# Kernel tuning notes

Measured on AMD Instinct MI355X. Metric: run time of the kernel, lower is better.

The kernel has to match this reference:

```python
import jax, jax.numpy as jnp
import numpy as np

L, B, S, H, V = 6, 8, 2048, 768, 32000
FF = 4 * H
EPS = 1e-5


def _ln(x, g, b):
    m = x.mean(-1, keepdims=True)
    v = ((x - m) ** 2).mean(-1, keepdims=True)
    return (x - m) / jnp.sqrt(v + EPS) * g + b


def setup_inputs() -> dict:
    key = jax.random.key(0)
    ks = iter(jax.random.split(key, 32))
    std = 0.02
    n = lambda shape: jax.random.normal(next(ks), shape, dtype=jnp.float32) * std
    inp = {
        'input_ids': jax.random.randint(next(ks), (B, S), 0, V, dtype=jnp.int64),
        'attention_mask': jnp.ones((B, S), dtype=jnp.int32),
        'tok_emb': n((V, H)),
        'pos_emb': n((S, H)),
        'Wq': n((L, H, H)), 'bq': n((L, H)),
        'Wk': n((L, H, H)), 'bk': n((L, H)),
        'Wv': n((L, H, H)), 'bv': n((L, H)),
        'Wo': n((L, H, H)), 'bo': n((L, H)),
        'ln1_g': jnp.ones((L, H), jnp.float32), 'ln1_b': jnp.zeros((L, H), jnp.float32),
        'ln2_g': jnp.ones((L, H), jnp.float32), 'ln2_b': jnp.zeros((L, H), jnp.float32),
        'W1': n((L, H, FF)), 'b1': n((L, FF)),
        'W2': n((L, FF, H)), 'b2': n((L, H)),
        'fln_g': jnp.ones((H,), jnp.float32), 'fln_b': jnp.zeros((H,), jnp.float32),
        'cls_W': n((H, 1)), 'cls_b': n((1,)),
    }
    return inp


def reference(input_ids, attention_mask, tok_emb, pos_emb, Wq, bq, Wk, bk, Wv, bv,
              Wo, bo, ln1_g, ln1_b, ln2_g, ln2_b, W1, b1, W2, b2,
              fln_g, fln_b, cls_W, cls_b):
    x = tok_emb[input_ids] + pos_emb[None, :S, :]  # [B,S,H]
    causal = jnp.triu(jnp.ones((S, S), dtype=bool), 1)  # True above diagonal
    pad = ~(attention_mask.astype(bool))[:, None, :]    # [B,1,S] True where padded
    full_mask = causal[None, :, :] | pad                # [B,S,S]
    scale = 1.0 / (H ** 0.5)
    for i in range(L):
        # --- attention block (pre-LN) ---
        h = _ln(x, ln1_g[i], ln1_b[i])
        q = h @ Wq[i] + bq[i]
        k = h @ Wk[i] + bk[i]
        v = h @ Wv[i] + bv[i]
        scores = jnp.einsum('bqd,bkd->bqk', q, k) * scale
        scores = jnp.where(full_mask, -jnp.inf, scores)
        attn = jax.nn.softmax(scores, axis=-1)
        o = jnp.einsum('bqk,bkd->bqd', attn, v) @ Wo[i] + bo[i]
        x = o + x
        # --- FFN block ---
        h = _ln(x, ln2_g[i], ln2_b[i])
        x = jax.nn.gelu(h @ W1[i] + b1[i], approximate=False) @ W2[i] + b2[i] + x
    x = _ln(x, fln_g, fln_b)
    # select hidden state of last non-padded token per row
    m = attention_mask.astype(jnp.int32)
    last = m.sum(1) - 1                      # [B]
    x_last = x[jnp.arange(B), last]          # [B,H]
    logits = x_last @ cls_W + cls_b          # [B,1]
    return logits
```

## Files before the change

### kernel.cpp

```cpp
#include <hip/hip_runtime.h>
#include <hip/hip_bf16.h>

#define Bn 8
#define Sn 2048
#define Hn 768
#define FFn 3072
#define Ln 6
#define BSn (Bn * Sn)
#define CQ 512
#define LN_EPS 1e-5f

typedef __hip_bfloat16 bf16;
typedef __bf16 bf16x8 __attribute__((ext_vector_type(8)));
typedef float f32x4 __attribute__((ext_vector_type(4)));

__device__ __forceinline__ float b2f(bf16 v) { return __bfloat162float(v); }
__device__ __forceinline__ void stc(float* p, float v) { *p = v; }
__device__ __forceinline__ void stc(bf16* p, float v) { *p = __float2bfloat16(v); }

union Pk8 { float4 v; bf16 h[8]; };

__device__ __forceinline__ void gld16(const bf16* g, short* l) {
  __builtin_amdgcn_global_load_lds(
      (const __attribute__((address_space(1))) unsigned int*)g,
      (__attribute__((address_space(3))) unsigned int*)l, 16, 0, 0);
}

__global__ void __launch_bounds__(256) embed_kernel(
    const int* __restrict__ ids, const float* __restrict__ tok,
    const float* __restrict__ pos, float* __restrict__ x) {
  long t = blockIdx.x;
  int s = (int)(t & (Sn - 1));
  long id = ids[t];
  const float* tr = tok + id * Hn;
  const float* pr = pos + (long)s * Hn;
  float* xr = x + t * Hn;
  for (int d = threadIdx.x; d < Hn; d += 256)
    xr[d] = tr[d] + pr[d];
}

__global__ void __launch_bounds__(256) transpose_cvt_kernel(
    const float* __restrict__ W, bf16* __restrict__ Wt, int K, int N) {
  __shared__ float t[32][33];
  int n0 = blockIdx.x * 32, k0 = blockIdx.y * 32;
  int tx = threadIdx.x & 31, ty = threadIdx.x >> 5;
#pragma unroll
  for (int i = 0; i < 32; i += 8)
    t[ty + i][tx] = W[(long)(k0 + ty + i) * N + n0 + tx];
  __syncthreads();
#pragma unroll
  for (int i = 0; i < 32; i += 8)
    stc(Wt + (long)(n0 + ty + i) * K + k0 + tx, t[tx][ty + i]);
}

__global__ void __launch_bounds__(256) ln_kernel(
    const float* __restrict__ x, const float* __restrict__ g,
    const float* __restrict__ b, bf16* __restrict__ out) {
  long token = blockIdx.x;
  const float* xr = x + token * Hn;
  bf16* orow = out + token * Hn;
  int tid = threadIdx.x;

  float vals[3];
  float s1 = 0.f;
#pragma unroll
  for (int i = 0; i < 3; i++) {
    vals[i] = xr[tid + 256 * i];
    s1 += vals[i];
  }
  __shared__ float sb[4];
  __shared__ float stat[2];
#pragma unroll
  for (int off = 32; off > 0; off >>= 1) s1 += __shfl_down(s1, off, 64);
  if ((tid & 63) == 0) sb[tid >> 6] = s1;
  __syncthreads();
  if (tid == 0) stat[0] = (sb[0] + sb[1] + sb[2] + sb[3]) * (1.0f / Hn);
  __syncthreads();
  float mean = stat[0];

  float s2 = 0.f;
#pragma unroll
  for (int i = 0; i < 3; i++) {
    float d = vals[i] - mean;
    s2 += d * d;
  }
#pragma unroll
  for (int off = 32; off > 0; off >>= 1) s2 += __shfl_down(s2, off, 64);
  if ((tid & 63) == 0) sb[tid >> 6] = s2;
  __syncthreads();
  if (tid == 0)
    stat[1] = rsqrtf((sb[0] + sb[1] + sb[2] + sb[3]) * (1.0f / Hn) + LN_EPS);
  __syncthreads();
  float inv = stat[1];

#pragma unroll
  for (int i = 0; i < 3; i++) {
    int d = tid + 256 * i;
    stc(orow + d, (vals[i] - mean) * inv * g[d] + b[d]);
  }
}

template <int EPI, typename CT>
__global__ void __launch_bounds__(256) mfma_gemm_kernel(
    const bf16* __restrict__ A, const bf16* __restrict__ Bt,
    const float* __restrict__ bias, const float* __restrict__ res,
    CT* __restrict__ C, int M, int N, int K) {
  __shared__ short As[128 * 32];
  __shared__ short Bs[128 * 32];
  int tid = threadIdx.x;
  int wave = tid >> 6, lane = tid & 63;
  int waveM = wave >> 1, waveN = wave & 1;
  int quad = lane >> 4, l16 = lane & 15;
  long rowBase = (long)blockIdx.y * 128;
  long colBase = (long)blockIdx.x * 128;
  const bf16* Ag = A + rowBase * K;
  const bf16* Bg = Bt + colBase * K;

  int srow = lane >> 2;
  int schunk = (lane & 3) * 8;

  f32x4 acc[4][4] = {};

  for (int kt = 0; kt < K; kt += 32) {
#pragma unroll
    for (int c = 0; c < 2; c++) {
      int r0 = wave * 32 + c * 16;
      gld16(Ag + (long)(r0 + srow) * K + kt + schunk, &As[r0 * 32]);
      gld16(Bg + (long)(r0 + srow) * K + kt + schunk, &Bs[r0 * 32]);
    }
    __syncthreads();

    bf16x8 af[4], bfr[4];
#pragma unroll
    for (int t = 0; t < 4; t++)
      af[t] = *(const bf16x8*)&As[(waveM * 64 + t * 16 + l16) * 32 + quad * 8];
#pragma unroll
    for (int u = 0; u < 4; u++)
      bfr[u] = *(const bf16x8*)&Bs[(waveN * 64 + u * 16 + l16) * 32 + quad * 8];
#pragma unroll
    for (int t = 0; t < 4; t++)
#pragma unroll
      for (int u = 0; u < 4; u++)
        acc[t][u] = __builtin_amdgcn_mfma_f32_16x16x32_bf16(af[t], bfr[u],
                                                            acc[t][u], 0, 0, 0);
    __syncthreads();
  }

#pragma unroll
  for (int t = 0; t < 4; t++) {
#pragma unroll
    for (int u = 0; u < 4; u++) {
      int col = (int)colBase + waveN * 64 + u * 16 + l16;
      float bv = bias[col];
      if (EPI == 3) {
        union { uint2 w; bf16 h[4]; } pk;
        long row0 = rowBase + waveM * 64 + t * 16 + quad * 4;
        long bb = row0 >> 11;
        long s = row0 & (Sn - 1);
#pragma unroll
        for (int r = 0; r < 4; r++)
          pk.h[r] = __float2bfloat16(acc[t][u][r] + bv);
        *reinterpret_cast<uint2*>((bf16*)C + (bb * Hn + col) * Sn + s) = pk.w;
      } else {
#pragma unroll
        for (int r = 0; r < 4; r++) {
          long row = rowBase + waveM * 64 + t * 16 + quad * 4 + r;
          float v = acc[t][u][r] + bv;
          if (EPI == 1) v += res[row * N + col];
          if (EPI == 2) v = 0.5f * v * (1.0f + erff(v * 0.70710678118654752f));
          stc(C + row * N + col, v);
        }
      }
    }
  }
}

__global__ void __launch_bounds__(256) qk_mfma_kernel(
    const bf16* __restrict__ q, const bf16* __restrict__ k,
    bf16* __restrict__ sc, int q0) {
  int kBase = blockIdx.x * 128;
  int qBase = q0 + blockIdx.y * 128;
  if (kBase > qBase + 127) return;
  int b = blockIdx.z;
  const bf16* Ag = q + ((long)b * Sn + qBase) * Hn;
  const bf16* Bg = k + ((long)b * Sn + kBase) * Hn;

  __shared__ short As[128 * 32];
  __shared__ short Bs[128 * 32];
  int tid = threadIdx.x;
  int wave = tid >> 6, lane = tid & 63;
  int waveM = wave >> 1, waveN = wave & 1;
  int quad = lane >> 4, l16 = lane & 15;
  int srow = lane >> 2;
  int schunk = (lane & 3) * 8;

  f32x4 acc[4][4] = {};

  for (int kt = 0; kt < Hn; kt += 32) {
#pragma unroll
    for (int c = 0; c < 2; c++) {
      int r0 = wave * 32 + c * 16;
      gld16(Ag + (long)(r0 + srow) * Hn + kt + schunk, &As[r0 * 32]);
      gld16(Bg + (long)(r0 + srow) * Hn + kt + schunk, &Bs[r0 * 32]);
    }
    __syncthreads();

    bf16x8 af[4], bfr[4];
#pragma unroll
    for (int t = 0; t < 4; t++)
      af[t] = *(const bf16x8*)&As[(waveM * 64 + t * 16 + l16) * 32 + quad * 8];
#pragma unroll
    for (int u = 0; u < 4; u++)
      bfr[u] = *(const bf16x8*)&Bs[(waveN * 64 + u * 16 + l16) * 32 + quad * 8];
#pragma unroll
    for (int t = 0; t < 4; t++)
#pragma unroll
      for (int u = 0; u < 4; u++)
        acc[t][u] = __builtin_amdgcn_mfma_f32_16x16x32_bf16(af[t], bfr[u],
                                                            acc[t][u], 0, 0, 0);
    __syncthreads();
  }

  const float scale = 0.03608439182435161f;
#pragma unroll
  for (int t = 0; t < 4; t++)
#pragma unroll
    for (int u = 0; u < 4; u++) {
      int col = kBase + waveN * 64 + u * 16 + l16;
#pragma unroll
      for (int r = 0; r < 4; r++) {
        long qRel = (long)(qBase - q0) + waveM * 64 + t * 16 + quad * 4 + r;
        stc(sc + ((long)b * CQ + qRel) * Sn + col, acc[t][u][r] * scale);
      }
    }
}

__global__ void __launch_bounds__(256) pv_mfma_kernel(
    const bf16* __restrict__ p, const bf16* __restrict__ vT,
    bf16* __restrict__ o, int q0) {
  int colBase = blockIdx.x * 128;
  int qBase = q0 + blockIdx.y * 128;
  int b = blockIdx.z;
  int klimit = qBase + 128;
  const bf16* Ag = p + ((long)b * CQ + (qBase - q0)) * Sn;
  const bf16* Bg = vT + ((long)b * Hn + colBase) * Sn;

  __shared__ short As[128 * 32];
  __shared__ short Bs[128 * 32];
  int tid = threadIdx.x;
  int wave = tid >> 6, lane = tid & 63;
  int waveM = wave >> 1, waveN = wave & 1;
  int quad = lane >> 4, l16 = lane & 15;
  int srow = lane >> 2;
  int schunk = (lane & 3) * 8;

  f32x4 acc[4][4] = {};

  for (int kt = 0; kt < klimit; kt += 32) {
#pragma unroll
    for (int c = 0; c < 2; c++) {
      int r0 = wave * 32 + c * 16;
      gld16(Ag + (long)(r0 + srow) * Sn + kt + schunk, &As[r0 * 32]);
      gld16(Bg + (long)(r0 + srow) * Sn + kt + schunk, &Bs[r0 * 32]);
    }
    __syncthreads();

    bf16x8 af[4], bfr[4];
#pragma unroll
    for (int t = 0; t < 4; t++)
      af[t] = *(const bf16x8*)&As[(waveM * 64 + t * 16 + l16) * 32 + quad * 8];
#pragma unroll
    for (int u = 0; u < 4; u++)
      bfr[u] = *(const bf16x8*)&Bs[(waveN * 64 + u * 16 + l16) * 32 + quad * 8];
#pragma unroll
    for (int t = 0; t < 4; t++)
#pragma unroll
      for (int u = 0; u < 4; u++)
        acc[t][u] = __builtin_amdgcn_mfma_f32_16x16x32_bf16(af[t], bfr[u],
                                                            acc[t][u], 0, 0, 0);
    __syncthreads();
  }

#pragma unroll
  for (int t = 0; t < 4; t++)
#pragma unroll
    for (int u = 0; u < 4; u++) {
      int col = colBase + waveN * 64 + u * 16 + l16;
#pragma unroll
      for (int r = 0; r < 4; r++) {
        long qAbs = (long)qBase + waveM * 64 + t * 16 + quad * 4 + r;
        stc(o + ((long)b * Sn + qAbs) * Hn + col, acc[t][u][r]);
      }
    }
}

__global__ void __launch_bounds__(256) softmax_kernel(
    bf16* __restrict__ sc, const int* __restrict__ mask, int q0) {
  int qRel = blockIdx.x;
  int b = blockIdx.y;
  int qg = q0 + qRel;
  bf16* row = sc + ((long)b * CQ + qRel) * Sn;
  const int* mrow = mask + b * Sn;
  int tid = threadIdx.x;
  int n = qg + 1;
  int limit = (qg & ~127) + 128;

  float sv[8];
  float lmax = -1e30f;
#pragma unroll
  for (int it = 0; it < 8; it++) {
    int kk = tid + it * 256;
    float s = -1e30f;
    if (kk < n) {
      s = b2f(row[kk]);
      if (mrow[kk] == 0) s = -1e30f;
    }
    sv[it] = s;
    lmax = fmaxf(lmax, s);
  }
  __shared__ float sb[4];
  __shared__ float stat;
#pragma unroll
  for (int off = 32; off > 0; off >>= 1)
    lmax = fmaxf(lmax, __shfl_down(lmax, off, 64));
  if ((tid & 63) == 0) sb[tid >> 6] = lmax;
  __syncthreads();
  if (tid == 0) stat = fmaxf(fmaxf(sb[0], sb[1]), fmaxf(sb[2], sb[3]));
  __syncthreads();
  float gmax = stat;

  float ev[8];
  float lsum = 0.f;
#pragma unroll
  for (int it = 0; it < 8; it++) {
    int kk = tid + it * 256;
    float e = 0.f;
    if (kk < n) e = __expf(sv[it] - gmax);
    ev[it] = e;
    lsum += e;
  }
#pragma unroll
  for (int off = 32; off > 0; off >>= 1) lsum += __shfl_down(lsum, off, 64);
  if ((tid & 63) == 0) sb[tid >> 6] = lsum;
  __syncthreads();
  if (tid == 0) stat = sb[0] + sb[1] + sb[2] + sb[3];
  __syncthreads();
  float inv = 1.0f / stat;

#pragma unroll
  for (int it = 0; it < 8; it++) {
    int kk = tid + it * 256;
    if (kk < n)
      stc(row + kk, ev[it] * inv);
    else if (kk < limit)
      stc(row + kk, 0.f);
  }
}

__global__ void __launch_bounds__(256) cls_kernel(
    const bf16* __restrict__ h, const int* __restrict__ mask,
    const float* __restrict__ clsW, const float* __restrict__ clsb,
    float* __restrict__ out) {
  int b = blockIdx.x;
  int tid = threadIdx.x;
  __shared__ float sb[4];
  __shared__ int ib[4];
  __shared__ int lastsh;

  int ls = 0;
  for (int s = tid; s < Sn; s += 256) ls += mask[b * Sn + s];
#pragma unroll
  for (int off = 32; off > 0; off >>= 1) ls += __shfl_down(ls, off, 64);
  if ((tid & 63) == 0) ib[tid >> 6] = ls;
  __syncthreads();
  if (tid == 0) lastsh = ib[0] + ib[1] + ib[2] + ib[3] - 1;
  __syncthreads();
  int last = lastsh;

  const bf16* row = h + ((long)b * Sn + last) * Hn;
  float acc = 0.f;
  for (int d = tid; d < Hn; d += 256) acc += b2f(row[d]) * clsW[d];
#pragma unroll
  for (int off = 32; off > 0; off >>= 1) acc += __shfl_down(acc, off, 64);
  if ((tid & 63) == 0) sb[tid >> 6] = acc;
  __syncthreads();
  if (tid == 0) out[b] = sb[0] + sb[1] + sb[2] + sb[3] + clsb[0];
}

extern "C" void kernel_launch(void* const* d_in, const int* in_sizes, int n_in,
                              void* d_out, int out_size, void* d_ws,
                              size_t ws_size, hipStream_t stream) {
  const int* ids     = (const int*)d_in[0];
  const int* mask    = (const int*)d_in[1];
  const float* tok   = (const float*)d_in[2];
  const float* pos   = (const float*)d_in[3];
  const float* Wq    = (const float*)d_in[4];
  const float* bq    = (const float*)d_in[5];
  const float* Wk    = (const float*)d_in[6];
  const float* bk    = (const float*)d_in[7];
  const float* Wv    = (const float*)d_in[8];
  const float* bv    = (const float*)d_in[9];
  const float* Wo    = (const float*)d_in[10];
  const float* bo    = (const float*)d_in[11];
  const float* ln1g  = (const float*)d_in[12];
  const float* ln1b  = (const float*)d_in[13];
  const float* ln2g  = (const float*)d_in[14];
  const float* ln2b  = (const float*)d_in[15];
  const float* W1    = (const float*)d_in[16];
  const float* b1    = (const float*)d_in[17];
  const float* W2    = (const float*)d_in[18];
  const float* b2    = (const float*)d_in[19];
  const float* flng  = (const float*)d_in[20];
  const float* flnb  = (const float*)d_in[21];
  const float* clsW  = (const float*)d_in[22];
  const float* clsb  = (const float*)d_in[23];

  float* x = (float*)d_ws;
  bf16* h  = (bf16*)(x + (size_t)BSn * Hn);
  bf16* cb = h + (size_t)BSn * Hn;
  bf16* qb = cb;
  bf16* kb = cb + (size_t)BSn * Hn;
  bf16* vtb = cb + 2 * (size_t)BSn * Hn;
  bf16* scb = cb + 3 * (size_t)BSn * Hn;
  bf16* wt = cb + (size_t)BSn * FFn;
  bf16* wqT = wt;
  bf16* wkT = wqT + (size_t)Hn * Hn;
  bf16* wvT = wkT + (size_t)Hn * Hn;
  bf16* woT = wvT + (size_t)Hn * Hn;
  bf16* w1T = woT + (size_t)Hn * Hn;
  bf16* w2T = w1T + (size_t)Hn * FFn;

  const int M = BSn;
  dim3 blk(256);
  dim3 gridH128(Hn / 128, M / 128);
  dim3 gridF128(FFn / 128, M / 128);
  dim3 gridQK(Sn / 128, CQ / 128, Bn);
  dim3 gridSM(CQ, Bn);
  dim3 gridPV(Hn / 128, CQ / 128, Bn);
  dim3 gridTH(Hn / 32, Hn / 32);
  dim3 gridT1(FFn / 32, Hn / 32);
  dim3 gridT2(Hn / 32, FFn / 32);

  embed_kernel<<<BSn, blk, 0, stream>>>(ids, tok, pos, x);

  for (int l = 0; l < Ln; l++) {
    const float* Wq_l = Wq + (size_t)l * Hn * Hn;
    const float* Wk_l = Wk + (size_t)l * Hn * Hn;
    const float* Wv_l = Wv + (size_t)l * Hn * Hn;
    const float* Wo_l = Wo + (size_t)l * Hn * Hn;
    const float* W1_l = W1 + (size_t)l * Hn * FFn;
    const float* W2_l = W2 + (size_t)l * FFn * Hn;

    transpose_cvt_kernel<<<gridTH, blk, 0, stream>>>(Wq_l, wqT, Hn, Hn);
    transpose_cvt_kernel<<<gridTH, blk, 0, stream>>>(Wk_l, wkT, Hn, Hn);
    transpose_cvt_kernel<<<gridTH, blk, 0, stream>>>(Wv_l, wvT, Hn, Hn);
    transpose_cvt_kernel<<<gridTH, blk, 0, stream>>>(Wo_l, woT, Hn, Hn);
    transpose_cvt_kernel<<<gridT1, blk, 0, stream>>>(W1_l, w1T, Hn, FFn);
    transpose_cvt_kernel<<<gridT2, blk, 0, stream>>>(W2_l, w2T, FFn, Hn);

    ln_kernel<<<BSn, blk, 0, stream>>>(x, ln1g + l * Hn, ln1b + l * Hn, h);
    mfma_gemm_kernel<0, bf16><<<gridH128, blk, 0, stream>>>(
        h, wqT, bq + l * Hn, nullptr, qb, M, Hn, Hn);
    mfma_gemm_kernel<0, bf16><<<gridH128, blk, 0, stream>>>(
        h, wkT, bk + l * Hn, nullptr, kb, M, Hn, Hn);
    mfma_gemm_kernel<3, bf16><<<gridH128, blk, 0, stream>>>(
        h, wvT, bv + l * Hn, nullptr, vtb, M, Hn, Hn);
    for (int c = 0; c < Sn / CQ; c++) {
      int q0 = c * CQ;
      qk_mfma_kernel<<<gridQK, blk, 0, stream>>>(qb, kb, scb, q0);
      softmax_kernel<<<gridSM, blk, 0, stream>>>(scb, mask, q0);
      pv_mfma_kernel<<<gridPV, blk, 0, stream>>>(scb, vtb, h, q0);
    }
    mfma_gemm_kernel<1, float><<<gridH128, blk, 0, stream>>>(
        h, woT, bo + l * Hn, x, x, M, Hn, Hn);

    ln_kernel<<<BSn, blk, 0, stream>>>(x, ln2g + l * Hn, ln2b + l * Hn, h);
    mfma_gemm_kernel<2, bf16><<<gridF128, blk, 0, stream>>>(
        h, w1T, b1 + l * FFn, nullptr, cb, M, FFn, Hn);
    mfma_gemm_kernel<1, float><<<gridH128, blk, 0, stream>>>(
        cb, w2T, b2 + l * Hn, x, x, M, Hn, FFn);
  }

  ln_kernel<<<BSn, blk, 0, stream>>>(x, flng, flnb, h);
  cls_kernel<<<Bn, blk, 0, stream>>>(h, mask, clsW, clsb, (float*)d_out);
}
```

Measured before the change: 4.729 ms.

## Fuse QKV GEMMs and weight transposes, add XCD-aware tile remap, vectorize softmax

Merges the six per-layer weight transpose launches into one kernel, and fuses the Q, K and V projections into a single GEMM over a concatenated transposed weight. The epilogue routes each output column range to the q, k or transposed-v buffer with the matching bias. GEMM launches switch to a 1D grid with a remap that gives each XCD a contiguous run of tiles, aiming for better L2 reuse. Softmax now loads and stores 8 bf16 values per thread with vector accesses. Risks are wrong offsets in the fused epilogue layout and added index arithmetic.

```diff
diff --git a/kernel.cpp b/kernel.cpp
--- a/kernel.cpp
+++ b/kernel.cpp
@@ -39,10 +39,35 @@
     xr[d] = tr[d] + pr[d];
 }
 
-__global__ void __launch_bounds__(256) transpose_cvt_kernel(
-    const float* __restrict__ W, bf16* __restrict__ Wt, int K, int N) {
+__global__ void __launch_bounds__(256) transpose_all_kernel(
+    const float* __restrict__ Wq_l, const float* __restrict__ Wk_l,
+    const float* __restrict__ Wv_l, const float* __restrict__ Wo_l,
+    const float* __restrict__ W1_l, const float* __restrict__ W2_l,
+    bf16* __restrict__ wt) {
+  int id = blockIdx.x;
+  const float* W;
+  bf16* Wt;
+  int K, N, tile, tilesX;
+  if (id < 2304) {
+    int w = id / 576;
+    tile = id - w * 576;
+    W = (w == 0) ? Wq_l : (w == 1) ? Wk_l : (w == 2) ? Wv_l : Wo_l;
+    Wt = wt + (size_t)w * Hn * Hn;
+    K = Hn; N = Hn; tilesX = Hn / 32;
+  } else if (id < 4608) {
+    tile = id - 2304;
+    W = W1_l;
+    Wt = wt + 4 * (size_t)Hn * Hn;
+    K = Hn; N = FFn; tilesX = FFn / 32;
+  } else {
+    tile = id - 4608;
+    W = W2_l;
+    Wt = wt + 4 * (size_t)Hn * Hn + (size_t)Hn * FFn;
+    K = FFn; N = Hn; tilesX = Hn / 32;
+  }
+  int n0 = (tile % tilesX) * 32, k0 = (tile / tilesX) * 32;
+
   __shared__ float t[32][33];
-  int n0 = blockIdx.x * 32, k0 = blockIdx.y * 32;
   int tx = threadIdx.x & 31, ty = threadIdx.x >> 5;
 #pragma unroll
   for (int i = 0; i < 32; i += 8)
@@ -104,15 +129,24 @@
 __global__ void __launch_bounds__(256) mfma_gemm_kernel(
     const bf16* __restrict__ A, const bf16* __restrict__ Bt,
     const float* __restrict__ bias, const float* __restrict__ res,
-    CT* __restrict__ C, int M, int N, int K) {
+    CT* __restrict__ C, int M, int N, int K,
+    const float* __restrict__ bias2, const float* __restrict__ bias3) {
   __shared__ short As[128 * 32];
   __shared__ short Bs[128 * 32];
   int tid = threadIdx.x;
   int wave = tid >> 6, lane = tid & 63;
   int waveM = wave >> 1, waveN = wave & 1;
   int quad = lane >> 4, l16 = lane & 15;
-  long rowBase = (long)blockIdx.y * 128;
-  long colBase = (long)blockIdx.x * 128;
+
+  int nwg = gridDim.x;
+  int orig = blockIdx.x;
+  int q8 = nwg >> 3, r8 = nwg & 7;
+  int xcd = orig & 7, loc = orig >> 3;
+  int wg = (xcd < r8 ? xcd * (q8 + 1) : r8 * (q8 + 1) + (xcd - r8) * q8) + loc;
+  int gx = N >> 7;
+  long colBase = (long)(wg % gx) * 128;
+  long rowBase = (long)(wg / gx) * 128;
+
   const bf16* Ag = A + rowBase * K;
   const bf16* Bg = Bt + colBase * K;
 
@@ -151,17 +185,28 @@
 #pragma unroll
     for (int u = 0; u < 4; u++) {
       int col = (int)colBase + waveN * 64 + u * 16 + l16;
-      float bv = bias[col];
-      if (EPI == 3) {
-        union { uint2 w; bf16 h[4]; } pk;
+      if (EPI == 4) {
         long row0 = rowBase + waveM * 64 + t * 16 + quad * 4;
-        long bb = row0 >> 11;
-        long s = row0 & (Sn - 1);
-#pragma unroll
-        for (int r = 0; r < 4; r++)
-          pk.h[r] = __float2bfloat16(acc[t][u][r] + bv);
-        *reinterpret_cast<uint2*>((bf16*)C + (bb * Hn + col) * Sn + s) = pk.w;
+        if (col < 1536) {
+          float bv = col < 768 ? bias[col] : bias2[col - 768];
+          bf16* dst = (bf16*)C + (col < 768 ? 0 : (size_t)BSn * Hn - Hn);
+#pragma unroll
+          for (int r = 0; r < 4; r++)
+            stc(dst + (row0 + r) * Hn + col, acc[t][u][r] + bv);
+        } else {
+          int vcol = col - 1536;
+          float bv = bias3[vcol];
+          union { uint2 w; bf16 h[4]; } pk;
+          long bb = row0 >> 11;
+          long s = row0 & (Sn - 1);
+#pragma unroll
+          for (int r = 0; r < 4; r++)
+            pk.h[r] = __float2bfloat16(acc[t][u][r] + bv);
+          bf16* vT = (bf16*)C + 2 * (size_t)BSn * Hn;
+          *reinterpret_cast<uint2*>(vT + (bb * Hn + vcol) * Sn + s) = pk.w;
+        }
       } else {
+        float bv = bias[col];
 #pragma unroll
         for (int r = 0; r < 4; r++) {
           long row = rowBase + waveM * 64 + t * 16 + quad * 4 + r;
@@ -304,18 +349,21 @@
   int tid = threadIdx.x;
   int n = qg + 1;
   int limit = (qg & ~127) + 128;
+  int k0 = tid * 8;
+
+  Pk8 pk;
+  pk.v = *reinterpret_cast<const float4*>(row + k0);
+  int4 m0 = *reinterpret_cast<const int4*>(mrow + k0);
+  int4 m1 = *reinterpret_cast<const int4*>(mrow + k0 + 4);
+  int mm[8] = {m0.x, m0.y, m0.z, m0.w, m1.x, m1.y, m1.z, m1.w};
 
   float sv[8];
   float lmax = -1e30f;
 #pragma unroll
-  for (int it = 0; it < 8; it++) {
-    int kk = tid + it * 256;
-    float s = -1e30f;
-    if (kk < n) {
-      s = b2f(row[kk]);
-      if (mrow[kk] == 0) s = -1e30f;
-    }
-    sv[it] = s;
+  for (int j = 0; j < 8; j++) {
+    int kk = k0 + j;
+    float s = (kk < n && mm[j] != 0) ? b2f(pk.h[j]) : -1e30f;
+    sv[j] = s;
     lmax = fmaxf(lmax, s);
   }
   __shared__ float sb[4];
@@ -332,11 +380,9 @@
   float ev[8];
   float lsum = 0.f;
 #pragma unroll
-  for (int it = 0; it < 8; it++) {
-    int kk = tid + it * 256;
-    float e = 0.f;
-    if (kk < n) e = __expf(sv[it] - gmax);
-    ev[it] = e;
+  for (int j = 0; j < 8; j++) {
+    float e = (sv[j] > -1e29f) ? __expf(sv[j] - gmax) : 0.f;
+    ev[j] = e;
     lsum += e;
   }
 #pragma unroll
@@ -347,13 +393,12 @@
   __syncthreads();
   float inv = 1.0f / stat;
 
-#pragma unroll
-  for (int it = 0; it < 8; it++) {
-    int kk = tid + it * 256;
-    if (kk < n)
-      stc(row + kk, ev[it] * inv);
-    else if (kk < limit)
-      stc(row + kk, 0.f);
+  if (k0 < limit) {
+    Pk8 o;
+#pragma unroll
+    for (int j = 0; j < 8; j++)
+      o.h[j] = __float2bfloat16((k0 + j < n) ? ev[j] * inv : 0.f);
+    *reinterpret_cast<float4*>(row + k0) = o.v;
   }
 }
 
@@ -424,22 +469,18 @@
   bf16* scb = cb + 3 * (size_t)BSn * Hn;
   bf16* wt = cb + (size_t)BSn * FFn;
   bf16* wqT = wt;
-  bf16* wkT = wqT + (size_t)Hn * Hn;
-  bf16* wvT = wkT + (size_t)Hn * Hn;
-  bf16* woT = wvT + (size_t)Hn * Hn;
+  bf16* woT = wqT + 3 * (size_t)Hn * Hn;
   bf16* w1T = woT + (size_t)Hn * Hn;
   bf16* w2T = w1T + (size_t)Hn * FFn;
 
   const int M = BSn;
   dim3 blk(256);
-  dim3 gridH128(Hn / 128, M / 128);
-  dim3 gridF128(FFn / 128, M / 128);
+  dim3 gridQKV(3 * 2304 / 3);
+  dim3 gridH1((Hn / 128) * (M / 128));
+  dim3 gridF1((FFn / 128) * (M / 128));
   dim3 gridQK(Sn / 128, CQ / 128, Bn);
   dim3 gridSM(CQ, Bn);
   dim3 gridPV(Hn / 128, CQ / 128, Bn);
-  dim3 gridTH(Hn / 32, Hn / 32);
-  dim3 gridT1(FFn / 32, Hn / 32);
-  dim3 gridT2(Hn / 32, FFn / 32);
 
   embed_kernel<<<BSn, blk, 0, stream>>>(ids, tok, pos, x);
 
@@ -451,34 +492,27 @@
     const float* W1_l = W1 + (size_t)l * Hn * FFn;
     const float* W2_l = W2 + (size_t)l * FFn * Hn;
 
-    transpose_cvt_kernel<<<gridTH, blk, 0, stream>>>(Wq_l, wqT, Hn, Hn);
-    transpose_cvt_kernel<<<gridTH, blk, 0, stream>>>(Wk_l, wkT, Hn, Hn);
-    transpose_cvt_kernel<<<gridTH, blk, 0, stream>>>(Wv_l, wvT, Hn, Hn);
-    transpose_cvt_kernel<<<gridTH, blk, 0, stream>>>(Wo_l, woT, Hn, Hn);
-    transpose_cvt_kernel<<<gridT1, blk, 0, stream>>>(W1_l, w1T, Hn, FFn);
-    transpose_cvt_kernel<<<gridT2, blk, 0, stream>>>(W2_l, w2T, FFn, Hn);
+    transpose_all_kernel<<<6912, blk, 0, stream>>>(Wq_l, Wk_l, Wv_l, Wo_l,
+                                                   W1_l, W2_l, wt);
 
     ln_kernel<<<BSn, blk, 0, stream>>>(x, ln1g + l * Hn, ln1b + l * Hn, h);
-    mfma_gemm_kernel<0, bf16><<<gridH128, blk, 0, stream>>>(
-        h, wqT, bq + l * Hn, nullptr, qb, M, Hn, Hn);
-    mfma_gemm_kernel<0, bf16><<<gridH128, blk, 0, stream>>>(
-        h, wkT, bk + l * Hn, nullptr, kb, M, Hn, Hn);
-    mfma_gemm_kernel<3, bf16><<<gridH128, blk, 0, stream>>>(
-        h, wvT, bv + l * Hn, nullptr, vtb, M, Hn, Hn);
+    mfma_gemm_kernel<4, bf16><<<dim3(18 * (M / 128)), blk, 0, stream>>>(
+        h, wqT, bq + l * Hn, nullptr, qb, M, 3 * Hn, Hn,
+        bk + l * Hn, bv + l * Hn);
     for (int c = 0; c < Sn / CQ; c++) {
       int q0 = c * CQ;
       qk_mfma_kernel<<<gridQK, blk, 0, stream>>>(qb, kb, scb, q0);
       softmax_kernel<<<gridSM, blk, 0, stream>>>(scb, mask, q0);
       pv_mfma_kernel<<<gridPV, blk, 0, stream>>>(scb, vtb, h, q0);
     }
-    mfma_gemm_kernel<1, float><<<gridH128, blk, 0, stream>>>(
-        h, woT, bo + l * Hn, x, x, M, Hn, Hn);
+    mfma_gemm_kernel<1, float><<<gridH1, blk, 0, stream>>>(
+        h, woT, bo + l * Hn, x, x, M, Hn, Hn, nullptr, nullptr);
 
     ln_kernel<<<BSn, blk, 0, stream>>>(x, ln2g + l * Hn, ln2b + l * Hn, h);
-    mfma_gemm_kernel<2, bf16><<<gridF128, blk, 0, stream>>>(
-        h, w1T, b1 + l * FFn, nullptr, cb, M, FFn, Hn);
-    mfma_gemm_kernel<1, float><<<gridH128, blk, 0, stream>>>(
-        cb, w2T, b2 + l * Hn, x, x, M, Hn, FFn);
+    mfma_gemm_kernel<2, bf16><<<gridF1, blk, 0, stream>>>(
+        h, w1T, b1 + l * FFn, nullptr, cb, M, FFn, Hn, nullptr, nullptr);
+    mfma_gemm_kernel<1, float><<<gridH1, blk, 0, stream>>>(
+        cb, w2T, b2 + l * Hn, x, x, M, Hn, FFn, nullptr, nullptr);
   }
 
   ln_kernel<<<BSn, blk, 0, stream>>>(x, flng, flnb, h);
```

Result: faster. 4.439 ms (-6.1%).
